# Kernel tuning notes

Measured on AMD Instinct MI355X. Metric: run time of the kernel, lower is better.

The kernel has to match this reference:

```python
import jax, jax.numpy as jnp
import numpy as np

N, E = 50000, 800000
DN, DE, H = 128, 64, 96


def _glorot(key, shape):
    fan_in = shape[0] if len(shape) > 1 else shape[0]
    return jax.random.normal(key, shape, jnp.float32) * (1.0 / np.sqrt(fan_in))


def setup_inputs() -> dict:
    key = jax.random.key(0)
    ks = jax.random.split(key, 24)
    inp = {
        "x": jax.random.normal(ks[0], (N, DN), jnp.float32),
        "edge_index": jax.random.randint(ks[1], (2, E), 0, N, jnp.int32),
        "edge_attr": jax.random.normal(ks[2], (E, DE), jnp.float32),
        # GATConv layer 0 (heads=1): lin [DN,H], lin_edge [DE,H], att vectors [H], bias [H]
        "w0": _glorot(ks[3], (DN, H)),
        "we0": _glorot(ks[4], (DE, H)),
        "as0": _glorot(ks[5], (H,)),
        "ad0": _glorot(ks[6], (H,)),
        "ae0": _glorot(ks[7], (H,)),
        "b0": jnp.zeros((H,), jnp.float32),
        # edge update 0: Linear(2H+DE -> H)
        "ew0": _glorot(ks[8], (2 * H + DE, H)),
        "eb0": jnp.zeros((H,), jnp.float32),
        # GATConv layer 1: lin [H,H], lin_edge [H,H]
        "w1": _glorot(ks[9], (H, H)),
        "we1": _glorot(ks[10], (H, H)),
        "as1": _glorot(ks[11], (H,)),
        "ad1": _glorot(ks[12], (H,)),
        "ae1": _glorot(ks[13], (H,)),
        "b1": jnp.zeros((H,), jnp.float32),
        # edge update 1: Linear(3H -> H)
        "ew1": _glorot(ks[14], (3 * H, H)),
        "eb1": jnp.zeros((H,), jnp.float32),
    }
    return inp


def gat_conv(x, src, dst, ea, W, We, a_s, a_d, a_e, b, n):
    """PyG GATConv, heads=1, eval mode, add_self_loops with fill_value='mean'."""
    ne = ea.shape[0]
    # self-loop edge attr = mean of incoming edge features per destination node
    cnt = jax.ops.segment_sum(jnp.ones((ne,), ea.dtype), dst, num_segments=n)
    loop_ea = jax.ops.segment_sum(ea, dst, num_segments=n) / jnp.maximum(cnt, 1.0)[:, None]
    ar = jnp.arange(n, dtype=src.dtype)
    sa = jnp.concatenate([src, ar])            # [E+N] augmented source idx
    da = jnp.concatenate([dst, ar])            # [E+N] augmented dest idx
    eaa = jnp.concatenate([ea, loop_ea], axis=0)
    h = x @ W                                   # [N,H]
    ep = eaa @ We                               # [E+N,H]
    logits = jax.nn.leaky_relu((h @ a_s)[sa] + (h @ a_d)[da] + ep @ a_e, 0.2)
    m = jax.ops.segment_max(logits, da, num_segments=n)
    p = jnp.exp(logits - m[da])
    denom = jax.ops.segment_sum(p, da, num_segments=n)
    alpha = p / denom[da]                       # segment softmax over dst neighborhoods
    return jax.ops.segment_sum(alpha[:, None] * h[sa], da, num_segments=n) + b


def reference(x, edge_index, edge_attr,
              w0, we0, as0, ad0, ae0, b0, ew0, eb0,
              w1, we1, as1, ad1, ae1, b1, ew1, eb1):
    src, dst = edge_index[0], edge_index[1]
    n = x.shape[0]
    # layer 0
    x = gat_conv(x, src, dst, edge_attr, w0, we0, as0, ad0, ae0, b0, n)
    edge_attr = jnp.concatenate([x[src], x[dst], edge_attr], axis=1) @ ew0 + eb0
    # layer 1
    x = gat_conv(x, src, dst, edge_attr, w1, we1, as1, ad1, ae1, b1, n)
    edge_attr = jnp.concatenate([x[src], x[dst], edge_attr], axis=1) @ ew1 + eb1
    return (x, edge_attr)
```

## Files before the change

kernel.cpp:

```cpp
#include <hip/hip_runtime.h>
#include <math.h>

#define NN 50000
#define NE 800000
#define DNODE 128
#define DEDGE 64
#define HD 96

__device__ __forceinline__ float lrelu(float x){ return x > 0.f ? x : 0.2f*x; }

__global__ void k_count(const int* __restrict__ dst, int* __restrict__ cnt){
  int e = blockIdx.x*256 + threadIdx.x;
  if (e < NE) atomicAdd(&cnt[dst[e]], 1);
}

__global__ __launch_bounds__(1024) void k_scan(const int* __restrict__ cnt,
                                               int* __restrict__ rowptr){
  __shared__ int sm[1024];
  __shared__ int run_s;
  int t = threadIdx.x;
  if (t == 0) run_s = 0;
  __syncthreads();
  const int nch = (NN + 1023)/1024;
  for (int c=0;c<nch;c++){
    int i = c*1024 + t;
    int v = (i < NN) ? cnt[i] : 0;
    sm[t] = v;
    __syncthreads();
    for (int off=1; off<1024; off<<=1){
      int add = (t >= off) ? sm[t-off] : 0;
      __syncthreads();
      sm[t] += add;
      __syncthreads();
    }
    if (i < NN) rowptr[i] = run_s + sm[t] - v;
    int total = sm[1023];
    __syncthreads();
    if (t == 0) run_s += total;
    __syncthreads();
  }
  if (t == 0) rowptr[NN] = run_s;
}

__global__ void k_fill(const int* __restrict__ src, const int* __restrict__ dst,
                       const int* __restrict__ rowptr, int* __restrict__ fillc,
                       int* __restrict__ perm, int* __restrict__ src_s){
  int e = blockIdx.x*256 + threadIdx.x;
  if (e >= NE) return;
  int d = dst[e];
  int pos = rowptr[d] + atomicAdd(&fillc[d], 1);
  perm[pos]  = e;
  src_s[pos] = src[e];
}

__global__ void k_vec(const float* __restrict__ We, const float* __restrict__ ae,
                      float* __restrict__ v, int K){
  int k = threadIdx.x;
  if (k < K){
    float s = 0.f;
    for (int j=0;j<HD;j++) s += We[k*HD + j]*ae[j];
    v[k] = s;
  }
}

__global__ void k_elr(const float* __restrict__ Ein, const float* __restrict__ v,
                      float* __restrict__ elr, int K){
  int e = blockIdx.x*256 + threadIdx.x;
  if (e >= NE) return;
  const float4* row = (const float4*)(Ein + (size_t)e*K);
  float s = 0.f;
  for (int k=0;k<K/4;k++){
    float4 a = row[k];
    float4 b = ((const float4*)v)[k];
    s += a.x*b.x + a.y*b.y + a.z*b.z + a.w*b.w;
  }
  elr[e] = s;
}

__global__ void k_sloop(const int* __restrict__ rowptr, const int* __restrict__ perm,
                        const float* __restrict__ elr, float* __restrict__ slp){
  int n = blockIdx.x*256 + threadIdx.x;
  if (n >= NN) return;
  int b = rowptr[n], e = rowptr[n+1];
  float s = 0.f;
  for (int i=b;i<e;i++) s += elr[perm[i]];
  slp[n] = s / fmaxf((float)(e-b), 1.f);
}

__global__ void k_dots(const float* __restrict__ h, const float* __restrict__ va,
                       const float* __restrict__ vb, float* __restrict__ hs,
                       float* __restrict__ hd){
  int n = blockIdx.x*256 + threadIdx.x;
  if (n >= NN) return;
  const float4* row = (const float4*)(h + (size_t)n*HD);
  float s1=0.f, s2=0.f;
  #pragma unroll
  for (int k=0;k<HD/4;k++){
    float4 a = row[k];
    float4 u = ((const float4*)va)[k];
    float4 w = ((const float4*)vb)[k];
    s1 += a.x*u.x + a.y*u.y + a.z*u.z + a.w*u.w;
    s2 += a.x*w.x + a.y*w.y + a.z*w.z + a.w*w.w;
  }
  hs[n]=s1; hd[n]=s2;
}

__global__ __launch_bounds__(256) void k_nodegemm(const float* __restrict__ X,
    const float* __restrict__ W, const float* __restrict__ bias,
    float* __restrict__ Y, int M, int K){
  __shared__ float Wl[DNODE*HD];
  for (int idx=threadIdx.x; idx<K*HD; idx+=256) Wl[idx] = W[idx];
  __syncthreads();
  int r  = threadIdx.x >> 3;
  int c0 = (threadIdx.x & 7)*12;
  int row = blockIdx.x*32 + r;
  if (row >= M) return;
  float acc[12];
  #pragma unroll
  for (int j=0;j<12;j++) acc[j]=0.f;
  const float* xr = X + (size_t)row*K;
  for (int k=0;k<K;k+=4){
    float4 xv = *(const float4*)(xr + k);
    float xs[4] = {xv.x, xv.y, xv.z, xv.w};
    #pragma unroll
    for (int kk=0;kk<4;kk++){
      const float* wr = Wl + (k+kk)*HD + c0;
      #pragma unroll
      for (int j=0;j<12;j++) acc[j] += xs[kk]*wr[j];
    }
  }
  float* yr = Y + (size_t)row*HD + c0;
  if (bias){
    #pragma unroll
    for (int j=0;j<12;j++) yr[j] = acc[j] + bias[c0+j];
  } else {
    #pragma unroll
    for (int j=0;j<12;j++) yr[j] = acc[j];
  }
}

__global__ __launch_bounds__(256) void k_edgegemm(const float* __restrict__ Ein,
    const float* __restrict__ W, int K,
    const float* __restrict__ A, const float* __restrict__ B,
    const int* __restrict__ src, const int* __restrict__ dst,
    const float* __restrict__ bias, float* __restrict__ Out){
  __shared__ float Wl[HD*HD];
  for (int idx=threadIdx.x; idx<K*HD; idx+=256) Wl[idx] = W[idx];
  __syncthreads();
  int r  = threadIdx.x >> 3;
  int c0 = (threadIdx.x & 7)*12;
  int e = blockIdx.x*32 + r;
  bool valid = e < NE;
  float acc[12];
  #pragma unroll
  for (int j=0;j<12;j++) acc[j]=0.f;
  if (valid){
    const float* er = Ein + (size_t)e*K;
    for (int k=0;k<K;k+=4){
      float4 xv = *(const float4*)(er + k);
      float xs[4]={xv.x,xv.y,xv.z,xv.w};
      #pragma unroll
      for (int kk=0;kk<4;kk++){
        const float* wr = Wl + (k+kk)*HD + c0;
        #pragma unroll
        for (int j=0;j<12;j++) acc[j] += xs[kk]*wr[j];
      }
    }
  }
  __syncthreads();
  if (!valid) return;
  int s = src[e], d = dst[e];
  const float* Ar = A + (size_t)s*HD + c0;
  const float* Br = B + (size_t)d*HD + c0;
  float* orow = Out + (size_t)e*HD + c0;
  #pragma unroll
  for (int j=0;j<12;j++) orow[j] = acc[j] + Ar[j] + Br[j] + bias[c0+j];
}

__global__ __launch_bounds__(256) void k_gat(const int* __restrict__ rowptr,
    const int* __restrict__ src_s, const int* __restrict__ perm,
    const float* __restrict__ hs, const float* __restrict__ hd,
    const float* __restrict__ elr, const float* __restrict__ slp,
    const float* __restrict__ h, const float* __restrict__ bias,
    float* __restrict__ Out){
  int lane = threadIdx.x & 63;
  int n = blockIdx.x*4 + (threadIdx.x >> 6);
  if (n >= NN) return;
  int beg = rowptr[n], end = rowptr[n+1];
  float hdn = hd[n];
  float selfL = lrelu(hs[n] + hdn + slp[n]);
  float mx = selfL;
  for (int i = beg + lane; i < end; i += 64)
    mx = fmaxf(mx, lrelu(hs[src_s[i]] + hdn + elr[perm[i]]));
  #pragma unroll
  for (int o=32;o>0;o>>=1) mx = fmaxf(mx, __shfl_xor(mx, o, 64));
  float acc0 = 0.f, acc1 = 0.f, denom = 0.f;
  for (int i = beg; i < end; ++i){
    int s = src_s[i];
    float p = __expf(lrelu(hs[s] + hdn + elr[perm[i]]) - mx);
    denom += p;
    acc0 += p * h[(size_t)s*HD + lane];
    if (lane < 32) acc1 += p * h[(size_t)s*HD + 64 + lane];
  }
  float ps = __expf(selfL - mx);
  denom += ps;
  acc0 += ps * h[(size_t)n*HD + lane];
  if (lane < 32) acc1 += ps * h[(size_t)n*HD + 64 + lane];
  float inv = 1.f/denom;
  Out[(size_t)n*HD + lane] = acc0*inv + bias[lane];
  if (lane < 32) Out[(size_t)n*HD + 64 + lane] = acc1*inv + bias[64+lane];
}

extern "C" void kernel_launch(void* const* d_in, const int* in_sizes, int n_in,
                              void* d_out, int out_size, void* d_ws, size_t ws_size,
                              hipStream_t stream){
  const float* x   = (const float*)d_in[0];
  const int*   ei  = (const int*)d_in[1];
  const float* ea  = (const float*)d_in[2];
  const float* w0  = (const float*)d_in[3];
  const float* we0 = (const float*)d_in[4];
  const float* as0 = (const float*)d_in[5];
  const float* ad0 = (const float*)d_in[6];
  const float* ae0 = (const float*)d_in[7];
  const float* b0  = (const float*)d_in[8];
  const float* ew0 = (const float*)d_in[9];
  const float* eb0 = (const float*)d_in[10];
  const float* w1  = (const float*)d_in[11];
  const float* we1 = (const float*)d_in[12];
  const float* as1 = (const float*)d_in[13];
  const float* ad1 = (const float*)d_in[14];
  const float* ae1 = (const float*)d_in[15];
  const float* b1  = (const float*)d_in[16];
  const float* ew1 = (const float*)d_in[17];
  const float* eb1 = (const float*)d_in[18];

  const int* srcp = ei;
  const int* dstp = ei + NE;

  char* ws = (char*)d_ws;
  size_t off = 0;
  auto carve = [&](size_t bytes)->char*{
    char* p = ws + off; off += (bytes + 255) & ~(size_t)255; return p;
  };
  int*   rowptr = (int*)carve(4ull*(NN+1));
  int*   fillc  = (int*)carve(4ull*NN);
  int*   perm   = (int*)carve(4ull*NE);
  int*   src_s  = (int*)carve(4ull*NE);
  float* hbuf   = (float*)carve(4ull*NN*HD);
  float* x0     = (float*)carve(4ull*NN*HD);
  float* Ab     = (float*)carve(4ull*NN*HD);
  float* Bb     = (float*)carve(4ull*NN*HD);
  float* hsb    = (float*)carve(4ull*NN);
  float* hdb    = (float*)carve(4ull*NN);
  float* slp    = (float*)carve(4ull*NN);
  float* elr    = (float*)carve(4ull*NE);
  float* vsm    = (float*)carve(4ull*128);
  (void)ws_size; (void)in_sizes; (void)n_in; (void)out_size;

  float* xout  = (float*)d_out;
  float* eaout = (float*)d_out + (size_t)NN*HD;

  const int EB = (NE + 255)/256;
  const int NB = (NN + 255)/256;

  hipMemsetAsync(fillc, 0, 4ull*NN, stream);
  k_count<<<EB, 256, 0, stream>>>(dstp, fillc);
  k_scan<<<1, 1024, 0, stream>>>(fillc, rowptr);
  hipMemsetAsync(fillc, 0, 4ull*NN, stream);
  k_fill<<<EB, 256, 0, stream>>>(srcp, dstp, rowptr, fillc, perm, src_s);

  k_vec<<<1, 128, 0, stream>>>(we0, ae0, vsm, DEDGE);
  k_elr<<<EB, 256, 0, stream>>>(ea, vsm, elr, DEDGE);
  k_sloop<<<NB, 256, 0, stream>>>(rowptr, perm, elr, slp);
  k_nodegemm<<<(NN+31)/32, 256, 0, stream>>>(x, w0, nullptr, hbuf, NN, DNODE);
  k_dots<<<NB, 256, 0, stream>>>(hbuf, as0, ad0, hsb, hdb);
  k_gat<<<(NN+3)/4, 256, 0, stream>>>(rowptr, src_s, perm, hsb, hdb, elr, slp, hbuf, b0, x0);

  k_nodegemm<<<(NN+31)/32, 256, 0, stream>>>(x0, ew0,           nullptr, Ab, NN, HD);
  k_nodegemm<<<(NN+31)/32, 256, 0, stream>>>(x0, ew0 + 96*HD,   nullptr, Bb, NN, HD);
  k_edgegemm<<<NE/32, 256, 0, stream>>>(ea, ew0 + 192*HD, DEDGE, Ab, Bb, srcp, dstp, eb0, eaout);

  k_vec<<<1, 128, 0, stream>>>(we1, ae1, vsm, HD);
  k_elr<<<EB, 256, 0, stream>>>(eaout, vsm, elr, HD);
  k_sloop<<<NB, 256, 0, stream>>>(rowptr, perm, elr, slp);
  k_nodegemm<<<(NN+31)/32, 256, 0, stream>>>(x0, w1, nullptr, hbuf, NN, HD);
  k_dots<<<NB, 256, 0, stream>>>(hbuf, as1, ad1, hsb, hdb);
  k_gat<<<(NN+3)/4, 256, 0, stream>>>(rowptr, src_s, perm, hsb, hdb, elr, slp, hbuf, b1, xout);

  k_nodegemm<<<(NN+31)/32, 256, 0, stream>>>(xout, ew1,         nullptr, Ab, NN, HD);
  k_nodegemm<<<(NN+31)/32, 256, 0, stream>>>(xout, ew1 + 96*HD, nullptr, Bb, NN, HD);
  k_edgegemm<<<NE/32, 256, 0, stream>>>(eaout, ew1 + 192*HD, HD, Ab, Bb, srcp, dstp, eb1, eaout);
}
```

Baseline: 2.116 ms.

## Fuse attention dots and self-loop means into GEMMs and register-tile rows

Node GEMMs now compute the source/destination attention dot products in their epilogue. The layer-1 edge GEMM also emits the edge logit term directly, removing the separate dots, elr and self-loop kernels. Both GEMMs process four rows per thread to reuse shared-memory weight loads across rows. The self-loop mean of edge logits is computed inside the GAT kernel during its max pass, and the single-block scan uses wavefront shuffles instead of a shared-memory Hillis-Steele loop. Larger per-thread tiles raise register pressure and may reduce occupancy.

```diff
diff --git a/kernel.cpp b/kernel.cpp
--- a/kernel.cpp
+++ b/kernel.cpp
@@ -16,30 +16,42 @@
 
 __global__ __launch_bounds__(1024) void k_scan(const int* __restrict__ cnt,
                                                int* __restrict__ rowptr){
-  __shared__ int sm[1024];
-  __shared__ int run_s;
-  int t = threadIdx.x;
-  if (t == 0) run_s = 0;
+  __shared__ int wsum[16];
+  __shared__ int carry_s;
+  const int t = threadIdx.x;
+  const int lane = t & 63, w = t >> 6;
+  if (t == 0) carry_s = 0;
   __syncthreads();
   const int nch = (NN + 1023)/1024;
   for (int c=0;c<nch;c++){
     int i = c*1024 + t;
     int v = (i < NN) ? cnt[i] : 0;
-    sm[t] = v;
+    int s = v;
+    #pragma unroll
+    for (int o=1;o<64;o<<=1){
+      int u = __shfl_up(s, o, 64);
+      if (lane >= o) s += u;
+    }
+    if (lane == 63) wsum[w] = s;
     __syncthreads();
-    for (int off=1; off<1024; off<<=1){
-      int add = (t >= off) ? sm[t-off] : 0;
-      __syncthreads();
-      sm[t] += add;
-      __syncthreads();
-    }
-    if (i < NN) rowptr[i] = run_s + sm[t] - v;
-    int total = sm[1023];
+    if (t < 16){
+      int x = wsum[t];
+      #pragma unroll
+      for (int o=1;o<16;o<<=1){
+        int u = __shfl_up(x, o, 64);
+        if (t >= o) x += u;
+      }
+      wsum[t] = x;
+    }
     __syncthreads();
-    if (t == 0) run_s += total;
+    int total = wsum[15];
+    int base = carry_s + (w ? wsum[w-1] : 0);
+    if (i < NN) rowptr[i] = base + s - v;
     __syncthreads();
-  }
-  if (t == 0) rowptr[NN] = run_s;
+    if (t == 0) carry_s += total;
+  }
+  __syncthreads();
+  if (t == 0) rowptr[NN] = carry_s;
 }
 
 __global__ void k_fill(const int* __restrict__ src, const int* __restrict__ dst,
@@ -77,110 +89,144 @@
   elr[e] = s;
 }
 
-__global__ void k_sloop(const int* __restrict__ rowptr, const int* __restrict__ perm,
-                        const float* __restrict__ elr, float* __restrict__ slp){
-  int n = blockIdx.x*256 + threadIdx.x;
-  if (n >= NN) return;
-  int b = rowptr[n], e = rowptr[n+1];
-  float s = 0.f;
-  for (int i=b;i<e;i++) s += elr[perm[i]];
-  slp[n] = s / fmaxf((float)(e-b), 1.f);
-}
-
-__global__ void k_dots(const float* __restrict__ h, const float* __restrict__ va,
-                       const float* __restrict__ vb, float* __restrict__ hs,
-                       float* __restrict__ hd){
-  int n = blockIdx.x*256 + threadIdx.x;
-  if (n >= NN) return;
-  const float4* row = (const float4*)(h + (size_t)n*HD);
-  float s1=0.f, s2=0.f;
-  #pragma unroll
-  for (int k=0;k<HD/4;k++){
-    float4 a = row[k];
-    float4 u = ((const float4*)va)[k];
-    float4 w = ((const float4*)vb)[k];
-    s1 += a.x*u.x + a.y*u.y + a.z*u.z + a.w*u.w;
-    s2 += a.x*w.x + a.y*w.y + a.z*w.z + a.w*w.w;
-  }
-  hs[n]=s1; hd[n]=s2;
-}
-
-__global__ __launch_bounds__(256) void k_nodegemm(const float* __restrict__ X,
-    const float* __restrict__ W, const float* __restrict__ bias,
-    float* __restrict__ Y, int M, int K){
-  __shared__ float Wl[DNODE*HD];
-  for (int idx=threadIdx.x; idx<K*HD; idx+=256) Wl[idx] = W[idx];
-  __syncthreads();
-  int r  = threadIdx.x >> 3;
-  int c0 = (threadIdx.x & 7)*12;
-  int row = blockIdx.x*32 + r;
-  if (row >= M) return;
-  float acc[12];
-  #pragma unroll
-  for (int j=0;j<12;j++) acc[j]=0.f;
-  const float* xr = X + (size_t)row*K;
+template<int K, bool DOTS>
+__global__ __launch_bounds__(256,4) void k_nodegemm_t(const float* __restrict__ X,
+    const float* __restrict__ W, float* __restrict__ Y, int M,
+    const float* __restrict__ va, const float* __restrict__ vb,
+    float* __restrict__ hs, float* __restrict__ hd){
+  __shared__ float Wl[K*HD];
+  for (int idx=threadIdx.x; idx<K*HD/4; idx+=256)
+    ((float4*)Wl)[idx] = ((const float4*)W)[idx];
+  __syncthreads();
+  const int r  = threadIdx.x >> 3;
+  const int c0 = (threadIdx.x & 7)*12;
+  const int r0 = blockIdx.x*128 + r;
+  float acc[4][12];
+  #pragma unroll
+  for (int q=0;q<4;q++)
+    #pragma unroll
+    for (int j=0;j<12;j++) acc[q][j]=0.f;
   for (int k=0;k<K;k+=4){
-    float4 xv = *(const float4*)(xr + k);
-    float xs[4] = {xv.x, xv.y, xv.z, xv.w};
+    float4 xv[4];
+    #pragma unroll
+    for (int q=0;q<4;q++){
+      int row = r0 + 32*q;
+      xv[q] = (row < M) ? *(const float4*)(X + (size_t)row*K + k)
+                        : make_float4(0.f,0.f,0.f,0.f);
+    }
     #pragma unroll
     for (int kk=0;kk<4;kk++){
+      float wv[12];
       const float* wr = Wl + (k+kk)*HD + c0;
       #pragma unroll
-      for (int j=0;j<12;j++) acc[j] += xs[kk]*wr[j];
-    }
-  }
-  float* yr = Y + (size_t)row*HD + c0;
-  if (bias){
-    #pragma unroll
-    for (int j=0;j<12;j++) yr[j] = acc[j] + bias[c0+j];
-  } else {
-    #pragma unroll
-    for (int j=0;j<12;j++) yr[j] = acc[j];
-  }
-}
-
-__global__ __launch_bounds__(256) void k_edgegemm(const float* __restrict__ Ein,
-    const float* __restrict__ W, int K,
+      for (int j=0;j<12;j++) wv[j] = wr[j];
+      #pragma unroll
+      for (int q=0;q<4;q++){
+        float xs = ((const float*)&xv[q])[kk];
+        #pragma unroll
+        for (int j=0;j<12;j++) acc[q][j] += xs*wv[j];
+      }
+    }
+  }
+  float vva[12], vvb[12];
+  if constexpr (DOTS){
+    #pragma unroll
+    for (int j=0;j<12;j++){ vva[j]=va[c0+j]; vvb[j]=vb[c0+j]; }
+  }
+  #pragma unroll
+  for (int q=0;q<4;q++){
+    int row = r0 + 32*q;
+    if (row >= M) continue;
+    float* yr = Y + (size_t)row*HD + c0;
+    float d1=0.f, d2=0.f;
+    #pragma unroll
+    for (int j=0;j<12;j++){
+      float o = acc[q][j];
+      yr[j] = o;
+      if constexpr (DOTS){ d1 += o*vva[j]; d2 += o*vvb[j]; }
+    }
+    if constexpr (DOTS){
+      #pragma unroll
+      for (int o=1;o<8;o<<=1){ d1 += __shfl_xor(d1,o,64); d2 += __shfl_xor(d2,o,64); }
+      if ((threadIdx.x&7)==0){ hs[row]=d1; hd[row]=d2; }
+    }
+  }
+}
+
+template<int K, bool ELR>
+__global__ __launch_bounds__(256,4) void k_edgegemm_t(const float* __restrict__ Ein,
+    const float* __restrict__ W,
     const float* __restrict__ A, const float* __restrict__ B,
     const int* __restrict__ src, const int* __restrict__ dst,
-    const float* __restrict__ bias, float* __restrict__ Out){
-  __shared__ float Wl[HD*HD];
-  for (int idx=threadIdx.x; idx<K*HD; idx+=256) Wl[idx] = W[idx];
-  __syncthreads();
-  int r  = threadIdx.x >> 3;
-  int c0 = (threadIdx.x & 7)*12;
-  int e = blockIdx.x*32 + r;
-  bool valid = e < NE;
-  float acc[12];
-  #pragma unroll
-  for (int j=0;j<12;j++) acc[j]=0.f;
-  if (valid){
-    const float* er = Ein + (size_t)e*K;
-    for (int k=0;k<K;k+=4){
-      float4 xv = *(const float4*)(er + k);
-      float xs[4]={xv.x,xv.y,xv.z,xv.w};
-      #pragma unroll
-      for (int kk=0;kk<4;kk++){
-        const float* wr = Wl + (k+kk)*HD + c0;
+    const float* __restrict__ bias, float* __restrict__ Out,
+    const float* __restrict__ v, float* __restrict__ elr){
+  __shared__ float Wl[K*HD];
+  for (int idx=threadIdx.x; idx<K*HD/4; idx+=256)
+    ((float4*)Wl)[idx] = ((const float4*)W)[idx];
+  __syncthreads();
+  const int r  = threadIdx.x >> 3;
+  const int c0 = (threadIdx.x & 7)*12;
+  const int e0 = blockIdx.x*128 + r;
+  float acc[4][12];
+  #pragma unroll
+  for (int q=0;q<4;q++)
+    #pragma unroll
+    for (int j=0;j<12;j++) acc[q][j]=0.f;
+  const float* e_base = Ein + (size_t)e0*K;
+  for (int k=0;k<K;k+=4){
+    float4 xv[4];
+    #pragma unroll
+    for (int q=0;q<4;q++)
+      xv[q] = *(const float4*)(e_base + (size_t)(32*q)*K + k);
+    #pragma unroll
+    for (int kk=0;kk<4;kk++){
+      float wv[12];
+      const float* wr = Wl + (k+kk)*HD + c0;
+      #pragma unroll
+      for (int j=0;j<12;j++) wv[j] = wr[j];
+      #pragma unroll
+      for (int q=0;q<4;q++){
+        float xs = ((const float*)&xv[q])[kk];
         #pragma unroll
-        for (int j=0;j<12;j++) acc[j] += xs[kk]*wr[j];
+        for (int j=0;j<12;j++) acc[q][j] += xs*wv[j];
       }
     }
   }
   __syncthreads();
-  if (!valid) return;
-  int s = src[e], d = dst[e];
-  const float* Ar = A + (size_t)s*HD + c0;
-  const float* Br = B + (size_t)d*HD + c0;
-  float* orow = Out + (size_t)e*HD + c0;
-  #pragma unroll
-  for (int j=0;j<12;j++) orow[j] = acc[j] + Ar[j] + Br[j] + bias[c0+j];
+  float bj[12], vv[12];
+  #pragma unroll
+  for (int j=0;j<12;j++) bj[j] = bias[c0+j];
+  if constexpr (ELR){
+    #pragma unroll
+    for (int j=0;j<12;j++) vv[j] = v[c0+j];
+  }
+  #pragma unroll
+  for (int q=0;q<4;q++){
+    int e = e0 + 32*q;
+    int s = src[e], d = dst[e];
+    const float* Ar = A + (size_t)s*HD + c0;
+    const float* Br = B + (size_t)d*HD + c0;
+    float* orow = Out + (size_t)e*HD + c0;
+    float pd = 0.f;
+    #pragma unroll
+    for (int j=0;j<12;j++){
+      float o = acc[q][j] + Ar[j] + Br[j] + bj[j];
+      orow[j] = o;
+      if constexpr (ELR) pd += o*vv[j];
+    }
+    if constexpr (ELR){
+      pd += __shfl_xor(pd,1,64);
+      pd += __shfl_xor(pd,2,64);
+      pd += __shfl_xor(pd,4,64);
+      if ((threadIdx.x&7)==0) elr[e] = pd;
+    }
+  }
 }
 
 __global__ __launch_bounds__(256) void k_gat(const int* __restrict__ rowptr,
     const int* __restrict__ src_s, const int* __restrict__ perm,
     const float* __restrict__ hs, const float* __restrict__ hd,
-    const float* __restrict__ elr, const float* __restrict__ slp,
+    const float* __restrict__ elr,
     const float* __restrict__ h, const float* __restrict__ bias,
     float* __restrict__ Out){
   int lane = threadIdx.x & 63;
@@ -188,12 +234,21 @@
   if (n >= NN) return;
   int beg = rowptr[n], end = rowptr[n+1];
   float hdn = hd[n];
-  float selfL = lrelu(hs[n] + hdn + slp[n]);
-  float mx = selfL;
-  for (int i = beg + lane; i < end; i += 64)
-    mx = fmaxf(mx, lrelu(hs[src_s[i]] + hdn + elr[perm[i]]));
-  #pragma unroll
-  for (int o=32;o>0;o>>=1) mx = fmaxf(mx, __shfl_xor(mx, o, 64));
+  float mxn = -INFINITY;
+  float se  = 0.f;
+  for (int i = beg + lane; i < end; i += 64){
+    float el = elr[perm[i]];
+    se += el;
+    mxn = fmaxf(mxn, lrelu(hs[src_s[i]] + hdn + el));
+  }
+  #pragma unroll
+  for (int o=32;o>0;o>>=1){
+    mxn = fmaxf(mxn, __shfl_xor(mxn, o, 64));
+    se += __shfl_xor(se, o, 64);
+  }
+  float slp = se / fmaxf((float)(end-beg), 1.f);
+  float selfL = lrelu(hs[n] + hdn + slp);
+  float mx = fmaxf(mxn, selfL);
   float acc0 = 0.f, acc1 = 0.f, denom = 0.f;
   for (int i = beg; i < end; ++i){
     int s = src_s[i];
@@ -252,16 +307,17 @@
   float* Bb     = (float*)carve(4ull*NN*HD);
   float* hsb    = (float*)carve(4ull*NN);
   float* hdb    = (float*)carve(4ull*NN);
-  float* slp    = (float*)carve(4ull*NN);
   float* elr    = (float*)carve(4ull*NE);
-  float* vsm    = (float*)carve(4ull*128);
+  float* vsm0   = (float*)carve(4ull*128);
+  float* vsm1   = (float*)carve(4ull*128);
   (void)ws_size; (void)in_sizes; (void)n_in; (void)out_size;
 
   float* xout  = (float*)d_out;
   float* eaout = (float*)d_out + (size_t)NN*HD;
 
-  const int EB = (NE + 255)/256;
-  const int NB = (NN + 255)/256;
+  const int EB  = (NE + 255)/256;
+  const int GE  = NE/128;
+  const int GN  = (NN + 127)/128;
 
   hipMemsetAsync(fillc, 0, 4ull*NN, stream);
   k_count<<<EB, 256, 0, stream>>>(dstp, fillc);
@@ -269,25 +325,23 @@
   hipMemsetAsync(fillc, 0, 4ull*NN, stream);
   k_fill<<<EB, 256, 0, stream>>>(srcp, dstp, rowptr, fillc, perm, src_s);
 
-  k_vec<<<1, 128, 0, stream>>>(we0, ae0, vsm, DEDGE);
-  k_elr<<<EB, 256, 0, stream>>>(ea, vsm, elr, DEDGE);
-  k_sloop<<<NB, 256, 0, stream>>>(rowptr, perm, elr, slp);
-  k_nodegemm<<<(NN+31)/32, 256, 0, stream>>>(x, w0, nullptr, hbuf, NN, DNODE);
-  k_dots<<<NB, 256, 0, stream>>>(hbuf, as0, ad0, hsb, hdb);
-  k_gat<<<(NN+3)/4, 256, 0, stream>>>(rowptr, src_s, perm, hsb, hdb, elr, slp, hbuf, b0, x0);
-
-  k_nodegemm<<<(NN+31)/32, 256, 0, stream>>>(x0, ew0,           nullptr, Ab, NN, HD);
-  k_nodegemm<<<(NN+31)/32, 256, 0, stream>>>(x0, ew0 + 96*HD,   nullptr, Bb, NN, HD);
-  k_edgegemm<<<NE/32, 256, 0, stream>>>(ea, ew0 + 192*HD, DEDGE, Ab, Bb, srcp, dstp, eb0, eaout);
-
-  k_vec<<<1, 128, 0, stream>>>(we1, ae1, vsm, HD);
-  k_elr<<<EB, 256, 0, stream>>>(eaout, vsm, elr, HD);
-  k_sloop<<<NB, 256, 0, stream>>>(rowptr, perm, elr, slp);
-  k_nodegemm<<<(NN+31)/32, 256, 0, stream>>>(x0, w1, nullptr, hbuf, NN, HD);
-  k_dots<<<NB, 256, 0, stream>>>(hbuf, as1, ad1, hsb, hdb);
-  k_gat<<<(NN+3)/4, 256, 0, stream>>>(rowptr, src_s, perm, hsb, hdb, elr, slp, hbuf, b1, xout);
-
-  k_nodegemm<<<(NN+31)/32, 256, 0, stream>>>(xout, ew1,         nullptr, Ab, NN, HD);
-  k_nodegemm<<<(NN+31)/32, 256, 0, stream>>>(xout, ew1 + 96*HD, nullptr, Bb, NN, HD);
-  k_edgegemm<<<NE/32, 256, 0, stream>>>(eaout, ew1 + 192*HD, HD, Ab, Bb, srcp, dstp, eb1, eaout);
-}
+  k_vec<<<1, 128, 0, stream>>>(we0, ae0, vsm0, DEDGE);
+  k_vec<<<1, 128, 0, stream>>>(we1, ae1, vsm1, HD);
+
+  k_elr<<<EB, 256, 0, stream>>>(ea, vsm0, elr, DEDGE);
+  k_nodegemm_t<DNODE,true><<<GN, 256, 0, stream>>>(x, w0, hbuf, NN, as0, ad0, hsb, hdb);
+  k_gat<<<(NN+3)/4, 256, 0, stream>>>(rowptr, src_s, perm, hsb, hdb, elr, hbuf, b0, x0);
+
+  k_nodegemm_t<HD,false><<<GN, 256, 0, stream>>>(x0, ew0,         Ab, NN, nullptr, nullptr, nullptr, nullptr);
+  k_nodegemm_t<HD,false><<<GN, 256, 0, stream>>>(x0, ew0 + 96*HD, Bb, NN, nullptr, nullptr, nullptr, nullptr);
+  k_edgegemm_t<DEDGE,true><<<GE, 256, 0, stream>>>(ea, ew0 + 192*HD, Ab, Bb, srcp, dstp,
+                                                   eb0, eaout, vsm1, elr);
+
+  k_nodegemm_t<HD,true><<<GN, 256, 0, stream>>>(x0, w1, hbuf, NN, as1, ad1, hsb, hdb);
+  k_gat<<<(NN+3)/4, 256, 0, stream>>>(rowptr, src_s, perm, hsb, hdb, elr, hbuf, b1, xout);
+
+  k_nodegemm_t<HD,false><<<GN, 256, 0, stream>>>(xout, ew1,         Ab, NN, nullptr, nullptr, nullptr, nullptr);
+  k_nodegemm_t<HD,false><<<GN, 256, 0, stream>>>(xout, ew1 + 96*HD, Bb, NN, nullptr, nullptr, nullptr, nullptr);
+  k_edgegemm_t<HD,false><<<GE, 256, 0, stream>>>(eaout, ew1 + 192*HD, Ab, Bb, srcp, dstp,
+                                                 eb1, eaout, nullptr, nullptr);
+}
```

Measured after the change: 1.733 ms. -18.1%, faster.
